# Kernel optimization log

Hardware: AMD Instinct MI355X
Metric: run time of the kernel (lower is better)

Reference implementation:

```python
import jax, jax.numpy as jnp
import numpy as np
from jax import lax

N = 2048


def setup_inputs() -> dict:
    key = jax.random.key(0)
    k1, k2, k3, k4 = jax.random.split(key, 4)
    root_logits = jax.random.normal(k1, (N,), jnp.float32)
    e = jax.random.normal(k2, (N, N), jnp.float32)
    # torch init zeros the diagonal of edge_probs
    edge_logits = e * (1.0 - jnp.eye(N, dtype=jnp.float32))
    # Gumbel noise made explicit so the reference is deterministic
    g_root = jax.random.gumbel(k3, (2, N), jnp.float32)
    g_edge = jax.random.gumbel(k4, (N, 2, N), jnp.float32)
    return {"root_logits": root_logits, "edge_logits": edge_logits,
            "g_root": g_root, "g_edge": g_edge}


def _sample_dag(root_logits, edge_logits, g_root, g_edge):
    n = root_logits.shape[0]
    f32 = jnp.float32
    i32 = jnp.int32

    # --- root sampling: hard gumbel-softmax over {root, not-root}, tau=1 ---
    yr = jnp.stack([jax.nn.log_sigmoid(root_logits),
                    jax.nn.log_sigmoid(-root_logits)]) + g_root  # [2, n]
    soft_r = jax.nn.softmax(yr, axis=0)[0]
    root_bool = yr[0] > yr[1]
    # straight-through: hard forward, soft gradient
    roots = root_bool.astype(f32) + soft_r - lax.stop_gradient(soft_r)

    # --- per-node edge sampling (noise pre-drawn; rows masked by BFS) ---
    ye = jnp.stack([jax.nn.log_sigmoid(edge_logits),
                    jax.nn.log_sigmoid(-edge_logits)], axis=1) + g_edge  # [n,2,n]
    soft_e = jax.nn.softmax(ye, axis=1)[:, 0, :]  # [n, n]
    hard_e = ye[:, 0, :] > ye[:, 1, :]            # [n, n] bool
    st_e = hard_e.astype(f32) + soft_e - lax.stop_gradient(soft_e)

    # --- FIFO queue init with roots in ascending index order ---
    idx = jnp.arange(n, dtype=i32)
    rank = jnp.cumsum(root_bool.astype(i32)) - 1
    pos = jnp.where(root_bool, rank, n)  # slot n is a write-only dump
    queue0 = jnp.zeros(n + 1, i32).at[pos].set(idx, mode='drop')
    tail0 = jnp.sum(root_bool).astype(i32)
    head0 = jnp.int32(0)
    dag0 = jnp.zeros((n, n), f32)
    anc0 = jnp.eye(n, dtype=bool)  # ancestors, anc[i,i]=1
    enq0 = root_bool               # dedup flag (equivalent to torch's pop-skip)

    def step(carry, _):
        dag, anc, queue, enq, head, tail = carry
        active = head < tail
        i = queue[head]
        anc_i = anc[i]  # includes i itself (eye init)
        cand = (1.0 - anc_i.astype(f32)) * (1.0 - roots)
        row = st_e[i] * cand
        dag = dag.at[i].set(jnp.where(active, row, dag[i]))
        children = hard_e[i] & (~anc_i) & (~root_bool) & active
        # anc[j] |= anc[i] | {i} for each child j (anc_i already contains i)
        anc = anc | (children[:, None] & anc_i[None, :])
        new = children & (~enq)
        r = jnp.cumsum(new.astype(i32)) - 1
        p = jnp.where(new, tail + r, n)
        queue = queue.at[p].set(idx, mode='drop')
        enq = enq | new
        tail = tail + jnp.sum(new).astype(i32)
        head = head + active.astype(i32)
        return (dag, anc, queue, enq, head, tail), None

    (dag, _, _, _, _, _), _ = lax.scan(
        step, (dag0, anc0, queue0, enq0, head0, tail0), None, length=n)
    return dag


def reference(root_logits, edge_logits, g_root, g_edge):
    return _sample_dag(root_logits, edge_logits, g_root, g_edge)
```

## Files before the change

### kernel.cpp

```cpp
#include <hip/hip_runtime.h>
#include <stdint.h>

typedef unsigned long long u64;
typedef unsigned int u32;
typedef unsigned short u16;

#define NN 2048
#define NW 32

#if __has_builtin(__builtin_amdgcn_sbfe)
#define SBFE(x, o) ((u32)__builtin_amdgcn_sbfe((int)(x), (u32)(o), 1u))
#else
#define SBFE(x, o) ((u32)(-(int)(((x) >> (o)) & 1u)))
#endif

static __device__ __forceinline__ bool gumbel_gt(float x, float g0, float g1) {
    float L = log1pf(expf(-fabsf(x)));
    float a = (-(fmaxf(-x, 0.f) + L)) + g0;
    float b = (-(fmaxf( x, 0.f) + L)) + g1;
    return a > b;
}

static __device__ __forceinline__ u64 orsel2(u64 acc, u64 w0, u64 w1, u64 m, int b0) {
    u32 mm = (b0 < 32) ? (u32)m : (u32)(m >> 32);
    int sh = b0 & 31;
    u32 s0 = SBFE(mm, sh);
    u32 s1 = SBFE(mm, sh + 1);
    u32 al = (u32)acc | ((u32)w0 & s0) | ((u32)w1 & s1);
    u32 ah = (u32)(acc >> 32) | ((u32)(w0 >> 32) & s0) | ((u32)(w1 >> 32) & s1);
    return ((u64)ah << 32) | al;
}

__global__ __launch_bounds__(256) void prep_kernel(
    const float* __restrict__ edge_logits,
    const float* __restrict__ g_edge,
    u64* __restrict__ heBits)
{
    const int i = blockIdx.x;
    const int t = threadIdx.x;
    const int lane = t & 63;
    const int wave = t >> 6;
    for (int c = wave; c < NW; c += 4) {
        int j = (c << 6) + lane;
        float x  = edge_logits[(size_t)i * NN + j];
        float g0 = g_edge[(size_t)i * (2 * NN) + j];
        float g1 = g_edge[(size_t)i * (2 * NN) + NN + j];
        u64 m = __ballot(gumbel_gt(x, g0, g1));
        if (lane == 0) heBits[(size_t)i * NW + c] = m;
    }
}

static __device__ void order_body(char* smem,
    const float* __restrict__ root_logits, const float* __restrict__ g_root,
    const u64* __restrict__ heBits,
    u16* __restrict__ posr, u16* __restrict__ porderW, int* __restrict__ nrPtr)
{
    int* s_porder = (int*)smem;
    int* s_cnt    = (int*)(smem + 8192);
    u64 (*s_U)[NW]  = (u64(*)[NW])(smem + 16384);
    u64 (*s_Pg)[NW] = (u64(*)[NW])(smem + 20480);
    u16* s_pos = (u16*)(smem + 24576);
    u16* s_f   = (u16*)(smem + 28672);
    u16* s_rk  = (u16*)(smem + 32768);
    u64* s_root = (u64*)(smem + 36864);
    u64* s_enq  = (u64*)(smem + 37120);
    u64* s_F    = (u64*)(smem + 37376);
    int* s_wsum = (int*)(smem + 37632);
    int* s_woff = (int*)(smem + 37696);
    int* s_sc   = (int*)(smem + 37760);
    int &s_base = s_sc[0]; int &s_lo = s_sc[1]; int &s_levcnt = s_sc[2];
    int &s_newcnt = s_sc[3]; int &s_nr = s_sc[4];

    const int t    = threadIdx.x;
    const int lane = t & 63;
    const int wid  = t >> 6;
    const int half = lane >> 5;
    const int w    = lane & 31;

    for (int p = 0; p < 2; ++p) {
        int j = p * 1024 + t;
        bool rb = gumbel_gt(root_logits[j], g_root[j], g_root[NN + j]);
        u64 m = __ballot(rb);
        if (lane == 0) s_root[j >> 6] = m;
    }
    __syncthreads();
    for (int p = 0; p < 2; ++p) {
        int j = p * 1024 + t;
        int ww = j >> 6; u64 bit = 1ull << (j & 63);
        if (s_root[ww] & bit) {
            int r = 0;
            for (int k = 0; k < ww; ++k) r += __popcll(s_root[k]);
            r += __popcll(s_root[ww] & (bit - 1ull));
            s_pos[j] = (u16)r;
            s_porder[r] = j;
        }
    }
    if (t < NW) s_enq[t] = s_root[t];
    if (t == 0) {
        int tl = 0;
        for (int k = 0; k < NW; ++k) tl += __popcll(s_root[k]);
        s_lo = 0; s_levcnt = tl; s_base = tl; s_nr = tl;
    }
    __syncthreads();

    while (s_levcnt > 0 && s_base < NN) {
        const int lo = s_lo, cnt = s_levcnt, base = s_base;
        const int seglen = (cnt + 15) >> 4;
        const int s0 = wid * seglen;
        const int s1 = (s0 + seglen < cnt) ? (s0 + seglen) : cnt;

        {
            u64 acc = 0;
            for (int m = s0 + half; m < s1; m += 2)
                acc |= heBits[(size_t)s_porder[lo + m] * NW + w];
            acc |= __shfl(acc, lane ^ 32);
            if (half == 0) s_U[wid][w] = acc;
        }
        __syncthreads();
        if (t < NW) {
            u64 o = 0;
            #pragma unroll
            for (int s = 0; s < 16; ++s) o |= s_U[s][t];
            s_F[t] = o & ~s_enq[t] & ~s_root[t];
        }
        __syncthreads();
        if (t < 512) {
            int s = t >> 5, ww = t & 31;
            u64 p = 0;
            for (int s2 = 0; s2 < s; ++s2) p |= s_U[s2][ww];
            s_Pg[s][ww] = p & s_F[ww];
        }
        __syncthreads();
        {
            u64 P  = s_Pg[wid][w];
            u64 Fw = s_F[w];
            int myidx = (s0 + lane < s1) ? s_porder[lo + s0 + lane] : 0;
            u64 rnext = 0;
            {
                int rowi0 = __shfl(myidx, half);
                if (s0 + half < s1) rnext = heBits[(size_t)rowi0 * NW + w];
            }
            for (int m = s0; m < s1; m += 2) {
                int m0 = m + half;
                u64 r = rnext;
                {
                    int sidx = (m + 2 - s0) + half;
                    if (sidx > 63) sidx = 0;
                    int rowin = __shfl(myidx, sidx);
                    rnext = 0;
                    if (m + 2 + half < s1) rnext = heBits[(size_t)rowin * NW + w];
                }
                u64 v = (m0 < s1) ? (r & Fw & ~P) : 0ull;
                u64 vlo = __shfl(v, w);
                u64 B = half ? (v & ~vlo) : v;
                int pc = __popcll(B);
                int inc = pc;
                #pragma unroll
                for (int d = 1; d < 32; d <<= 1) {
                    int u2 = __shfl_up(inc, d, 64);
                    if (w >= d) inc += u2;
                }
                int excl = inc - pc;
                int tot = __shfl(inc, (half << 5) | 31);
                if (w == 0 && m0 < s1) s_cnt[m0] = tot;
                u64 mm = B;
                int idx = excl;
                while (mm) {
                    int b = __ffsll(mm) - 1; mm &= mm - 1;
                    int j = (w << 6) + b;
                    s_f[j]  = (u16)m0;
                    s_rk[j] = (u16)idx++;
                }
                P |= B | __shfl(B, lane ^ 32);
            }
        }
        __syncthreads();
        {
            int b0 = 2 * t, b1 = 2 * t + 1;
            int c0 = (b0 < cnt) ? s_cnt[b0] : 0;
            int c1 = (b1 < cnt) ? s_cnt[b1] : 0;
            int pairv = c0 + c1;
            int incl = pairv;
            for (int d = 1; d < 64; d <<= 1) {
                int v = __shfl_up(incl, d, 64);
                if (lane >= d) incl += v;
            }
            if (lane == 63) s_wsum[wid] = incl;
            __syncthreads();
            if (t < 16) {
                int v = s_wsum[t];
                int inc2 = v;
                for (int d = 1; d < 16; d <<= 1) {
                    int u = __shfl_up(inc2, d, 16);
                    if (t >= d) inc2 += u;
                }
                s_woff[t] = inc2 - v;
                if (t == 15) s_newcnt = inc2;
            }
            __syncthreads();
            int excl = s_woff[wid] + (incl - pairv);
            if (b0 < cnt) s_cnt[b0] = excl;
            if (b1 < cnt) s_cnt[b1] = excl + c0;
        }
        __syncthreads();
        for (int p = 0; p < 2; ++p) {
            int j = p * 1024 + t;
            int ww = j >> 6;
            if ((s_F[ww] >> (j & 63)) & 1ull) {
                int slot = base + s_cnt[s_f[j]] + s_rk[j];
                s_pos[j] = (u16)slot;
                s_porder[slot] = j;
            }
        }
        if (t < NW) s_enq[t] |= s_F[t];
        __syncthreads();
        if (t == 0) { s_lo = base; s_levcnt = s_newcnt; s_base = base + s_newcnt; }
        __syncthreads();
    }

    for (int p = 0; p < 2; ++p) {
        int j = p * 1024 + t;
        int ww = j >> 6; u64 bit = 1ull << (j & 63);
        if (!((s_enq[ww] >> (j & 63)) & 1ull)) {
            int rk = 0;
            for (int k2 = 0; k2 < ww; ++k2) rk += __popcll(~s_enq[k2]);
            rk += __popcll(~s_enq[ww] & (bit - 1ull));
            int slot = s_base + rk;
            s_pos[j] = (u16)slot;
            s_porder[slot] = j;
        }
    }
    __syncthreads();
    for (int p = 0; p < 2; ++p) {
        int j = p * 1024 + t;
        int fl = s_pos[j];
        if ((s_root[j >> 6] >> (j & 63)) & 1ull) fl |= 0x8000;
        if ((s_enq[j >> 6]  >> (j & 63)) & 1ull) fl |= 0x4000;
        posr[j] = (u16)fl;
        porderW[j] = (u16)s_porder[j];
    }
    if (t == 0) *nrPtr = s_nr;
}

__global__ __launch_bounds__(1024) void ordtrans_kernel(
    const float* __restrict__ root_logits,
    const float* __restrict__ g_root,
    const u64* __restrict__ heBits,
    u64* __restrict__ heT,
    u16* __restrict__ posr,
    u16* __restrict__ porderW,
    int* __restrict__ nrPtr)
{
    __shared__ __align__(16) char smem[38016];
    const int bid  = blockIdx.x;
    const int t    = threadIdx.x;
    const int lane = t & 63;
    const int wv   = t >> 6;

    if (bid == 0) {
        order_body(smem, root_logits, g_root, heBits, posr, porderW, nrPtr);
    } else {
        int gw = (bid - 1) * 16 + wv;
        if (gw < 1024) {
            int ti = gw >> 5, tj = gw & 31;
            u64 w = heBits[(size_t)(64 * ti + lane) * NW + tj];
            u64 out = 0;
            #pragma unroll
            for (int b = 0; b < 64; ++b) {
                u64 m = __ballot(((w >> b) & 1ull) != 0);
                if (b == lane) out = m;
            }
            heT[(size_t)(64 * tj + lane) * NW + ti] = out;
        }
    }
}

__global__ __launch_bounds__(256) void apbuild_kernel(
    const u64* __restrict__ heT, const u16* __restrict__ porderW,
    const int* __restrict__ nrPtr, u64* __restrict__ Ap)
{
    __shared__ u64 s_row[NW];
    __shared__ u16 s_inv[NN];
    __shared__ int s_invb, s_nr;
    const int b = blockIdx.x;
    const int t = threadIdx.x;
    for (int q = t; q < NN; q += 256) s_inv[q] = porderW[q];
    if (t == 0) { s_invb = porderW[b]; s_nr = *nrPtr; }
    __syncthreads();
    if (t < NW) s_row[t] = heT[(size_t)s_invb * NW + t];
    __syncthreads();
    const bool bge = (b >= s_nr);
    for (int pass = 0; pass < 8; ++pass) {
        int a = pass * 256 + t;
        int ia = s_inv[a];
        bool bit = bge && (a < b) &&
                   (((s_row[ia >> 6] >> (ia & 63)) & 1ull) != 0);
        u64 m = __ballot(bit);
        if ((t & 63) == 0) Ap[(size_t)b * NW + (a >> 6)] = m;
    }
}

__global__ __launch_bounds__(64) void diagap2_kernel(
    u64* __restrict__ Ap, u64* __restrict__ Di)
{
    const int i = blockIdx.x;
    const int j = blockIdx.y;
    if (j > i) return;
    __shared__ u64 sm[64];
    const int r = threadIdx.x;
    u64 M = Ap[(size_t)(64 * i + r) * NW + i] | (1ull << r);
    for (int s = 0; s < 6; ++s) {
        sm[r] = M;
        __syncthreads();
        u64 acc = 0;
        #pragma unroll
        for (int b = 0; b < 64; ++b)
            acc |= sm[b] & (0ull - ((M >> b) & 1ull));
        __syncthreads();
        M = acc;
    }
    if (j == i) { Di[64 * i + r] = M; return; }
    sm[r] = Ap[(size_t)(64 * i + r) * NW + j];
    __syncthreads();
    u64 acc = 0;
    #pragma unroll
    for (int b = 0; b < 64; ++b)
        acc |= sm[b] & (0ull - ((M >> b) & 1ull));
    Ap[(size_t)(64 * i + r) * NW + j] = acc;
}

__global__ __launch_bounds__(1024) void colhalf_kernel(
    const u64* __restrict__ Ap, const u64* __restrict__ Di,
    u64* __restrict__ Anc)
{
    __shared__ __align__(16) u64 colA[16][64];
    __shared__ u64 part[16][64];
    const int t  = threadIdx.x;
    const int r  = t & 63;
    const int wv = t >> 6;
    const int k    = blockIdx.x & 15;
    const int hb   = blockIdx.x >> 4;
    const int base = hb << 4;
    const int bend = base + 16;
    const int kk   = base + k;

    for (int row = t; row < 64 * kk; row += 1024)
        Anc[(size_t)row * NW + kk] = 0ull;

    if (t < 64) {
        u64 d = Di[64 * kk + r];
        colA[0][r] = d;
        Anc[(size_t)(64 * kk + r) * NW + kk] = d;
    }
    __syncthreads();

    const int j0 = kk + wv;

    for (int ib = kk + 1; ib < bend; ib += 4) {
        u64 m0[4], acc[4];
        #pragma unroll
        for (int g = 0; g < 4; ++g) {
            int ig = ib + g;
            bool v = (ig < bend);
            m0[g] = (v && (j0 < ib)) ? Ap[(size_t)(64 * ig + r) * NW + j0] : 0ull;
            acc[g] = 0ull;
        }
        u64 tm[3][3];
        #pragma unroll
        for (int s = 0; s < 3; ++s) {
            #pragma unroll
            for (int q = 0; q < 3; ++q) {
                int g = s + 1 + q;
                tm[s][q] = (g < 4 && (ib + g) < bend)
                    ? Ap[(size_t)(64 * (ib + g) + r) * NW + (ib + s)] : 0ull;
            }
        }

        if (j0 < ib) {
            const ulonglong2* rp = (const ulonglong2*)&colA[j0 - kk][0];
            #pragma unroll
            for (int bp = 0; bp < 32; ++bp) {
                ulonglong2 ww = rp[bp];
                #pragma unroll
                for (int g = 0; g < 4; ++g)
                    acc[g] = orsel2(acc[g], ww.x, ww.y, m0[g], 2 * bp);
            }
        }

        #pragma unroll
        for (int s = 0; s < 4; ++s) {
            const int i = ib + s;
            if (i < bend) {
                part[wv][r] = acc[s];
                __syncthreads();
                if (wv < 2) {
                    u64 red = part[0][r];
                    #pragma unroll
                    for (int p = 1; p < 16; ++p) red |= part[p][r];
                    if (wv == 0) colA[i - kk][r] = red;
                    else Anc[(size_t)(64 * i + r) * NW + kk] = red;
                }
                __syncthreads();
                if (s < 3 && (i + 1) < bend) {
                    const u64* rowp = colA[i - kk];
                    #pragma unroll
                    for (int bi = 0; bi < 4; ++bi) {
                        int b = 4 * wv + bi;
                        u64 w = rowp[b];
                        u32 wl = (u32)w, wh = (u32)(w >> 32);
                        #pragma unroll
                        for (int q = 0; q < 3; ++q) {
                            int g = s + 1 + q;
                            if (g < 4) {
                                u32 sm2 = (u32)(0u - (u32)((tm[s][q] >> b) & 1ull));
                                u32 al = (u32)acc[g] | (wl & sm2);
                                u32 ah = (u32)(acc[g] >> 32) | (wh & sm2);
                                acc[g] = ((u64)ah << 32) | al;
                            }
                        }
                    }
                }
            }
        }
    }
}

__global__ __launch_bounds__(256) void mergefused_kernel(
    const u64* __restrict__ Bstar,
    const u64* __restrict__ Cp,
    const u64* __restrict__ Astar,
    u64* __restrict__ Out)
{
    __shared__ u64 SQ[256][17];
    __shared__ u64 PL[8][16];
    __shared__ u64 YL[8][16];
    const int t    = threadIdx.x;
    const int lane = t & 63;
    const int wv   = t >> 6;
    const int grp  = lane >> 4;
    const int w    = lane & 15;
    const int rb   = blockIdx.x;

    if (t < 128) PL[t >> 4][t & 15] = Bstar[(size_t)(8 * rb + (t >> 4)) * NW + (t & 15)];

    u64 acc0 = 0, acc1 = 0;

    for (int cs = 0; cs < 4; ++cs) {
        __syncthreads();
        for (int q = t; q < 4096; q += 256)
            SQ[q >> 4][q & 15] = Cp[(size_t)(256 * cs + (q >> 4)) * NW + (q & 15)];
        __syncthreads();
        #pragma unroll
        for (int cw = 0; cw < 4; ++cw) {
            u64 m0 = PL[2 * wv + 0][cs * 4 + cw];
            u64 m1 = PL[2 * wv + 1][cs * 4 + cw];
            #pragma unroll
            for (int cc = 0; cc < 16; ++cc) {
                u64 qq = SQ[cw * 64 + cc * 4 + grp][w];
                int sh = (cc & 7) * 4 + grp;
                u32 h0 = (cc < 8) ? (u32)m0 : (u32)(m0 >> 32);
                u32 h1 = (cc < 8) ? (u32)m1 : (u32)(m1 >> 32);
                u32 ql = (u32)qq, qh = (u32)(qq >> 32);
                u32 s;
                s = SBFE(h0, sh);
                acc0 = ((u64)(((u32)(acc0 >> 32)) | (qh & s)) << 32) | (((u32)acc0) | (ql & s));
                s = SBFE(h1, sh);
                acc1 = ((u64)(((u32)(acc1 >> 32)) | (qh & s)) << 32) | (((u32)acc1) | (ql & s));
            }
        }
    }
    acc0 |= __shfl_xor(acc0, 16); acc0 |= __shfl_xor(acc0, 32);
    acc1 |= __shfl_xor(acc1, 16); acc1 |= __shfl_xor(acc1, 32);
    if (grp == 0) { YL[2 * wv + 0][w] = acc0; YL[2 * wv + 1][w] = acc1; }
    __syncthreads();

    acc0 = 0; acc1 = 0;
    for (int cs = 0; cs < 4; ++cs) {
        __syncthreads();
        for (int q = t; q < 4096; q += 256)
            SQ[q >> 4][q & 15] = Astar[(size_t)(256 * cs + (q >> 4)) * NW + (q & 15)];
        __syncthreads();
        #pragma unroll
        for (int cw = 0; cw < 4; ++cw) {
            u64 m0 = YL[2 * wv + 0][cs * 4 + cw];
            u64 m1 = YL[2 * wv + 1][cs * 4 + cw];
            #pragma unroll
            for (int cc = 0; cc < 16; ++cc) {
                u64 qq = SQ[cw * 64 + cc * 4 + grp][w];
                int sh = (cc & 7) * 4 + grp;
                u32 h0 = (cc < 8) ? (u32)m0 : (u32)(m0 >> 32);
                u32 h1 = (cc < 8) ? (u32)m1 : (u32)(m1 >> 32);
                u32 ql = (u32)qq, qh = (u32)(qq >> 32);
                u32 s;
                s = SBFE(h0, sh);
                acc0 = ((u64)(((u32)(acc0 >> 32)) | (qh & s)) << 32) | (((u32)acc0) | (ql & s));
                s = SBFE(h1, sh);
                acc1 = ((u64)(((u32)(acc1 >> 32)) | (qh & s)) << 32) | (((u32)acc1) | (ql & s));
            }
        }
    }
    acc0 |= __shfl_xor(acc0, 16); acc0 |= __shfl_xor(acc0, 32);
    acc1 |= __shfl_xor(acc1, 16); acc1 |= __shfl_xor(acc1, 32);
    if (grp == 0) {
        size_t base = (size_t)(8 * rb + 2 * wv) * NW + w;
        Out[base] = acc0;
        Out[base + NW] = acc1;
    }
}

__global__ __launch_bounds__(256) void foldout_kernel(
    const u64* __restrict__ heBits,
    const u64* __restrict__ Anc,
    const u16* __restrict__ posr,
    float* __restrict__ dag)
{
    __shared__ u64 s_anc[NW];
    __shared__ u64 s_he[NW];
    __shared__ u16 s_pr[NN];
    const int i = blockIdx.x;
    const int t = threadIdx.x;

    ((int4*)s_pr)[t] = ((const int4*)posr)[t];
    __syncthreads();
    const int fl = s_pr[i];
    const int pi = fl & 0x7FF;
    if (t < NW) {
        s_anc[t] = Anc[(size_t)pi * NW + t];
        s_he[t]  = heBits[(size_t)i * NW + t];
    }
    __syncthreads();
    const bool reach_i = (fl & 0x4000) != 0;
    const int j0 = t * 8;
    float o[8];
    #pragma unroll
    for (int e = 0; e < 8; ++e) {
        int j = j0 + e;
        int pr = s_pr[j];
        int a = pr & 0x7FF;
        bool he = ((s_he[j >> 6] >> (j & 63)) & 1ull) != 0;
        bool anc = ((s_anc[a >> 6] >> (a & 63)) & 1ull) != 0;
        o[e] = (reach_i && he && ((pr & 0x8000) == 0) && !anc) ? 1.f : 0.f;
    }
    float4* outp = (float4*)(dag + (size_t)i * NN + j0);
    outp[0] = make_float4(o[0], o[1], o[2], o[3]);
    outp[1] = make_float4(o[4], o[5], o[6], o[7]);
}

extern "C" void kernel_launch(void* const* d_in, const int* in_sizes, int n_in,
                              void* d_out, int out_size, void* d_ws, size_t ws_size,
                              hipStream_t stream) {
    const float* root_logits = (const float*)d_in[0];
    const float* edge_logits = (const float*)d_in[1];
    const float* g_root      = (const float*)d_in[2];
    const float* g_edge      = (const float*)d_in[3];
    float* dag = (float*)d_out;

    char* ws = (char*)d_ws;
    u64* heBits  = (u64*)(ws);
    u64* heT     = (u64*)(ws + (512 << 10));
    u64* Ap      = (u64*)(ws + (1 << 20));
    u64* Anc     = (u64*)(ws + (1 << 20) + (512 << 10));
    u64* Di      = (u64*)(ws + (2 << 20));
    u16* posr    = (u16*)(ws + (2 << 20) + (192 << 10));
    u16* porderW = (u16*)(ws + (2 << 20) + (196 << 10));
    int* nrPtr   = (int*)(ws + (2 << 20) + (200 << 10));

    prep_kernel    <<<NN, 256, 0, stream>>>(edge_logits, g_edge, heBits);
    ordtrans_kernel<<<256, 1024, 0, stream>>>(root_logits, g_root, heBits, heT,
                                              posr, porderW, nrPtr);
    apbuild_kernel <<<NN, 256, 0, stream>>>(heT, porderW, nrPtr, Ap);
    diagap2_kernel <<<dim3(NW, NW), 64, 0, stream>>>(Ap, Di);
    colhalf_kernel <<<NW, 1024, 0, stream>>>(Ap, Di, Anc);
    mergefused_kernel<<<128, 256, 0, stream>>>(Anc + (size_t)1024 * NW + 16,
                                               Ap + (size_t)1024 * NW,
                                               Anc,
                                               Anc + (size_t)1024 * NW);
    foldout_kernel <<<NN, 256, 0, stream>>>(heBits, Anc, posr, dag);
}
```

Measured before the change: 154.5 us.

## Split fused merge into two K-split kernels with partial-OR reduction in consumers

The single merge kernel, which ran 128 blocks that each looped serially over four column chunks for two chained boolean products, is replaced by two kernels launched on a 128x4 grid. Each block handles one K-chunk and writes a partial result. The partials are OR-reduced by the next consumer (merge2 or foldout) instead of being written back into Anc. This gives four times the blocks and parallelism at the cost of an extra launch, extra partial-buffer traffic, and a conditional path in foldout.

```diff
diff --git a/kernel.cpp b/kernel.cpp
--- a/kernel.cpp
+++ b/kernel.cpp
@@ -425,92 +425,110 @@
     }
 }
 
-__global__ __launch_bounds__(256) void mergefused_kernel(
+__global__ __launch_bounds__(256) void merge1_kernel(
     const u64* __restrict__ Bstar,
-    const u64* __restrict__ Cp,
-    const u64* __restrict__ Astar,
-    u64* __restrict__ Out)
+    const u64* __restrict__ CpRows,
+    u64* __restrict__ Yp)
 {
     __shared__ u64 SQ[256][17];
-    __shared__ u64 PL[8][16];
-    __shared__ u64 YL[8][16];
+    __shared__ u64 PL[8][4];
     const int t    = threadIdx.x;
     const int lane = t & 63;
     const int wv   = t >> 6;
     const int grp  = lane >> 4;
     const int w    = lane & 15;
     const int rb   = blockIdx.x;
-
-    if (t < 128) PL[t >> 4][t & 15] = Bstar[(size_t)(8 * rb + (t >> 4)) * NW + (t & 15)];
+    const int q    = blockIdx.y;
+
+    if (t < 32)
+        PL[t >> 2][t & 3] = Bstar[(size_t)(8 * rb + (t >> 2)) * NW + 16 + 4 * q + (t & 3)];
+    for (int s = t; s < 4096; s += 256)
+        SQ[s >> 4][s & 15] = CpRows[(size_t)(256 * q + (s >> 4)) * NW + (s & 15)];
+    __syncthreads();
 
     u64 acc0 = 0, acc1 = 0;
-
-    for (int cs = 0; cs < 4; ++cs) {
-        __syncthreads();
-        for (int q = t; q < 4096; q += 256)
-            SQ[q >> 4][q & 15] = Cp[(size_t)(256 * cs + (q >> 4)) * NW + (q & 15)];
-        __syncthreads();
+    #pragma unroll
+    for (int cw = 0; cw < 4; ++cw) {
+        u64 m0 = PL[2 * wv + 0][cw];
+        u64 m1 = PL[2 * wv + 1][cw];
         #pragma unroll
-        for (int cw = 0; cw < 4; ++cw) {
-            u64 m0 = PL[2 * wv + 0][cs * 4 + cw];
-            u64 m1 = PL[2 * wv + 1][cs * 4 + cw];
-            #pragma unroll
-            for (int cc = 0; cc < 16; ++cc) {
-                u64 qq = SQ[cw * 64 + cc * 4 + grp][w];
-                int sh = (cc & 7) * 4 + grp;
-                u32 h0 = (cc < 8) ? (u32)m0 : (u32)(m0 >> 32);
-                u32 h1 = (cc < 8) ? (u32)m1 : (u32)(m1 >> 32);
-                u32 ql = (u32)qq, qh = (u32)(qq >> 32);
-                u32 s;
-                s = SBFE(h0, sh);
-                acc0 = ((u64)(((u32)(acc0 >> 32)) | (qh & s)) << 32) | (((u32)acc0) | (ql & s));
-                s = SBFE(h1, sh);
-                acc1 = ((u64)(((u32)(acc1 >> 32)) | (qh & s)) << 32) | (((u32)acc1) | (ql & s));
-            }
-        }
-    }
-    acc0 |= __shfl_xor(acc0, 16); acc0 |= __shfl_xor(acc0, 32);
-    acc1 |= __shfl_xor(acc1, 16); acc1 |= __shfl_xor(acc1, 32);
-    if (grp == 0) { YL[2 * wv + 0][w] = acc0; YL[2 * wv + 1][w] = acc1; }
-    __syncthreads();
-
-    acc0 = 0; acc1 = 0;
-    for (int cs = 0; cs < 4; ++cs) {
-        __syncthreads();
-        for (int q = t; q < 4096; q += 256)
-            SQ[q >> 4][q & 15] = Astar[(size_t)(256 * cs + (q >> 4)) * NW + (q & 15)];
-        __syncthreads();
-        #pragma unroll
-        for (int cw = 0; cw < 4; ++cw) {
-            u64 m0 = YL[2 * wv + 0][cs * 4 + cw];
-            u64 m1 = YL[2 * wv + 1][cs * 4 + cw];
-            #pragma unroll
-            for (int cc = 0; cc < 16; ++cc) {
-                u64 qq = SQ[cw * 64 + cc * 4 + grp][w];
-                int sh = (cc & 7) * 4 + grp;
-                u32 h0 = (cc < 8) ? (u32)m0 : (u32)(m0 >> 32);
-                u32 h1 = (cc < 8) ? (u32)m1 : (u32)(m1 >> 32);
-                u32 ql = (u32)qq, qh = (u32)(qq >> 32);
-                u32 s;
-                s = SBFE(h0, sh);
-                acc0 = ((u64)(((u32)(acc0 >> 32)) | (qh & s)) << 32) | (((u32)acc0) | (ql & s));
-                s = SBFE(h1, sh);
-                acc1 = ((u64)(((u32)(acc1 >> 32)) | (qh & s)) << 32) | (((u32)acc1) | (ql & s));
-            }
+        for (int cc = 0; cc < 16; ++cc) {
+            u64 qq = SQ[cw * 64 + cc * 4 + grp][w];
+            int sh = (cc & 7) * 4 + grp;
+            u32 h0 = (cc < 8) ? (u32)m0 : (u32)(m0 >> 32);
+            u32 h1 = (cc < 8) ? (u32)m1 : (u32)(m1 >> 32);
+            u32 ql = (u32)qq, qh = (u32)(qq >> 32);
+            u32 s;
+            s = SBFE(h0, sh);
+            acc0 = ((u64)(((u32)(acc0 >> 32)) | (qh & s)) << 32) | (((u32)acc0) | (ql & s));
+            s = SBFE(h1, sh);
+            acc1 = ((u64)(((u32)(acc1 >> 32)) | (qh & s)) << 32) | (((u32)acc1) | (ql & s));
         }
     }
     acc0 |= __shfl_xor(acc0, 16); acc0 |= __shfl_xor(acc0, 32);
     acc1 |= __shfl_xor(acc1, 16); acc1 |= __shfl_xor(acc1, 32);
     if (grp == 0) {
-        size_t base = (size_t)(8 * rb + 2 * wv) * NW + w;
-        Out[base] = acc0;
-        Out[base + NW] = acc1;
+        size_t base = ((size_t)q * 1024 + 8 * rb + 2 * wv) * 16 + w;
+        Yp[base] = acc0;
+        Yp[base + 16] = acc1;
+    }
+}
+
+__global__ __launch_bounds__(256) void merge2_kernel(
+    const u64* __restrict__ Yp,
+    const u64* __restrict__ Astar,
+    u64* __restrict__ Xp)
+{
+    __shared__ u64 SQ[256][17];
+    __shared__ u64 PL[8][4];
+    const int t    = threadIdx.x;
+    const int lane = t & 63;
+    const int wv   = t >> 6;
+    const int grp  = lane >> 4;
+    const int w    = lane & 15;
+    const int rb   = blockIdx.x;
+    const int q    = blockIdx.y;
+
+    if (t < 32) {
+        size_t idx = (size_t)(8 * rb + (t >> 2)) * 16 + 4 * q + (t & 3);
+        PL[t >> 2][t & 3] = Yp[idx] | Yp[idx + 16384] | Yp[idx + 32768] | Yp[idx + 49152];
+    }
+    for (int s = t; s < 4096; s += 256)
+        SQ[s >> 4][s & 15] = Astar[(size_t)(256 * q + (s >> 4)) * NW + (s & 15)];
+    __syncthreads();
+
+    u64 acc0 = 0, acc1 = 0;
+    #pragma unroll
+    for (int cw = 0; cw < 4; ++cw) {
+        u64 m0 = PL[2 * wv + 0][cw];
+        u64 m1 = PL[2 * wv + 1][cw];
+        #pragma unroll
+        for (int cc = 0; cc < 16; ++cc) {
+            u64 qq = SQ[cw * 64 + cc * 4 + grp][w];
+            int sh = (cc & 7) * 4 + grp;
+            u32 h0 = (cc < 8) ? (u32)m0 : (u32)(m0 >> 32);
+            u32 h1 = (cc < 8) ? (u32)m1 : (u32)(m1 >> 32);
+            u32 ql = (u32)qq, qh = (u32)(qq >> 32);
+            u32 s;
+            s = SBFE(h0, sh);
+            acc0 = ((u64)(((u32)(acc0 >> 32)) | (qh & s)) << 32) | (((u32)acc0) | (ql & s));
+            s = SBFE(h1, sh);
+            acc1 = ((u64)(((u32)(acc1 >> 32)) | (qh & s)) << 32) | (((u32)acc1) | (ql & s));
+        }
+    }
+    acc0 |= __shfl_xor(acc0, 16); acc0 |= __shfl_xor(acc0, 32);
+    acc1 |= __shfl_xor(acc1, 16); acc1 |= __shfl_xor(acc1, 32);
+    if (grp == 0) {
+        size_t base = ((size_t)q * 1024 + 8 * rb + 2 * wv) * 16 + w;
+        Xp[base] = acc0;
+        Xp[base + 16] = acc1;
     }
 }
 
 __global__ __launch_bounds__(256) void foldout_kernel(
     const u64* __restrict__ heBits,
     const u64* __restrict__ Anc,
+    const u64* __restrict__ Xp,
     const u16* __restrict__ posr,
     float* __restrict__ dag)
 {
@@ -525,7 +543,14 @@
     const int fl = s_pr[i];
     const int pi = fl & 0x7FF;
     if (t < NW) {
-        s_anc[t] = Anc[(size_t)pi * NW + t];
+        u64 v;
+        if (pi >= 1024 && t < 16) {
+            size_t idx = (size_t)(pi - 1024) * 16 + t;
+            v = Xp[idx] | Xp[idx + 16384] | Xp[idx + 32768] | Xp[idx + 49152];
+        } else {
+            v = Anc[(size_t)pi * NW + t];
+        }
+        s_anc[t] = v;
         s_he[t]  = heBits[(size_t)i * NW + t];
     }
     __syncthreads();
@@ -564,6 +589,8 @@
     u16* posr    = (u16*)(ws + (2 << 20) + (192 << 10));
     u16* porderW = (u16*)(ws + (2 << 20) + (196 << 10));
     int* nrPtr   = (int*)(ws + (2 << 20) + (200 << 10));
+    u64* Yp      = (u64*)(ws + (3 << 20));
+    u64* Xp      = (u64*)(ws + (3 << 20) + (512 << 10));
 
     prep_kernel    <<<NN, 256, 0, stream>>>(edge_logits, g_edge, heBits);
     ordtrans_kernel<<<256, 1024, 0, stream>>>(root_logits, g_root, heBits, heT,
@@ -571,9 +598,8 @@
     apbuild_kernel <<<NN, 256, 0, stream>>>(heT, porderW, nrPtr, Ap);
     diagap2_kernel <<<dim3(NW, NW), 64, 0, stream>>>(Ap, Di);
     colhalf_kernel <<<NW, 1024, 0, stream>>>(Ap, Di, Anc);
-    mergefused_kernel<<<128, 256, 0, stream>>>(Anc + (size_t)1024 * NW + 16,
-                                               Ap + (size_t)1024 * NW,
-                                               Anc,
-                                               Anc + (size_t)1024 * NW);
-    foldout_kernel <<<NN, 256, 0, stream>>>(heBits, Anc, posr, dag);
-}
+    merge1_kernel  <<<dim3(128, 4), 256, 0, stream>>>(Anc + (size_t)1024 * NW,
+                                                      Ap + (size_t)1024 * NW, Yp);
+    merge2_kernel  <<<dim3(128, 4), 256, 0, stream>>>(Yp, Anc, Xp);
+    foldout_kernel <<<NN, 256, 0, stream>>>(heBits, Anc, Xp, posr, dag);
+}
```

New measurement: 127.4 us (median of 2 runs). 1.21x faster.
